# Optimization experiments

Hardware: AMD Instinct MI355X
Metric: run time of the kernel (lower is better)

The kernel has to match this reference:

```python
import jax, jax.numpy as jnp
import numpy as np

EPS = 1e-20


def setup_inputs() -> dict:
    key = jax.random.key(0)
    k_u, k_w = jax.random.split(key)
    B, n_in, d_in, N, D = 128, 1152, 8, 32, 16
    u = jax.random.normal(k_u, (B, n_in, d_in), dtype=jnp.float32)
    # xavier_normal for W: fan_in = d_in, fan_out = D (last two dims)
    std = float(np.sqrt(2.0 / (d_in + D)))
    W = jax.random.normal(k_w, (n_in, N, d_in, D), dtype=jnp.float32) * std
    b = jnp.zeros((n_in, N), dtype=jnp.float32)
    return {"u": u, "W": W, "b": b}


def reference(u, W, b):
    # u: [B, i, n]; W: [i, j, n, m]; u_hat: [B, i, j, m]
    u_hat = jnp.einsum('ijnm,bin->bijm', W, u)
    # agreement score uses detached (stop-gradient) u_hat
    u_hat_d = jax.lax.stop_gradient(u_hat)
    D = W.shape[-1]
    a = jnp.einsum('bijm,bijm->bij', u_hat_d, u_hat_d) / jnp.sqrt(jnp.float32(D))
    # softmax over parent-capsule axis j, plus learned bias b[i, j]
    c = jax.nn.softmax(a, axis=2) + b[None, :, :]
    s = jnp.einsum('bij,bijm->bjm', c, u_hat)
    # squash nonlinearity
    n = jnp.linalg.norm(s, axis=-1, keepdims=True)
    v = (n * n / (1.0 + n * n) / (n + EPS)) * s
    return v
```

## Files before the change

### kernel.cpp

```cpp
#include <hip/hip_runtime.h>
#include <math.h>


#define NB 128
#define NI 1152
#define NJ 32
#define DM 16
#define JMSZ 512
#define BB 4
#define TPB 256
#define BPB ((TPB / 64) * BB)

template <int IC_, bool ATOMIC>
__global__ __launch_bounds__(TPB, 4) void caps_main(
    const float* __restrict__ u, const float* __restrict__ W,
    const float* __restrict__ bias, float* __restrict__ out, int nchunk) {
  const int chunk = blockIdx.x;
  const int bg = blockIdx.y;
  const int tid = threadIdx.x;
  const int wid = __builtin_amdgcn_readfirstlane(tid >> 6);
  const int lane = tid & 63;
  const int j = lane >> 1;
  const int h = lane & 1;
  const int b0 = __builtin_amdgcn_readfirstlane(bg * BPB + wid * BB);
  const int i0 = chunk * IC_;

  float acc[BB][8];
#pragma unroll
  for (int bb = 0; bb < BB; ++bb)
#pragma unroll
    for (int k = 0; k < 8; ++k) acc[bb][k] = 0.f;

  const char* wbase = (const char*)W + (size_t)i0 * 16384 + j * 512 + h * 32;

  for (int t = 0; t < IC_; ++t) {
    const int i = i0 + t;
    const char* wp = wbase + (size_t)t * 16384;

    float un[BB][8];
#pragma unroll
    for (int bb = 0; bb < BB; ++bb) {
      const float* up = u + ((size_t)(b0 + bb) * NI + i) * 8;
      float4 a0 = *(const float4*)up;
      float4 a1 = *(const float4*)(up + 4);
      un[bb][0] = a0.x; un[bb][1] = a0.y; un[bb][2] = a0.z; un[bb][3] = a0.w;
      un[bb][4] = a1.x; un[bb][5] = a1.y; un[bb][6] = a1.z; un[bb][7] = a1.w;
    }
    const float bj = bias[(size_t)i * NJ + j];

    float uh[BB][8];
#pragma unroll
    for (int bb = 0; bb < BB; ++bb)
#pragma unroll
      for (int k = 0; k < 8; ++k) uh[bb][k] = 0.f;

#pragma unroll
    for (int half = 0; half < 2; ++half) {
      float4 w0[4], w1[4];
#pragma unroll
      for (int nn = 0; nn < 4; ++nn) {
        const int n = half * 4 + nn;
        w0[nn] = *(const float4*)(wp + n * 64);
        w1[nn] = *(const float4*)(wp + n * 64 + 16);
      }
#pragma unroll
      for (int nn = 0; nn < 4; ++nn) {
        const int n = half * 4 + nn;
#pragma unroll
        for (int bb = 0; bb < BB; ++bb) {
          const float uv = un[bb][n];
          uh[bb][0] = fmaf(uv, w0[nn].x, uh[bb][0]);
          uh[bb][1] = fmaf(uv, w0[nn].y, uh[bb][1]);
          uh[bb][2] = fmaf(uv, w0[nn].z, uh[bb][2]);
          uh[bb][3] = fmaf(uv, w0[nn].w, uh[bb][3]);
          uh[bb][4] = fmaf(uv, w1[nn].x, uh[bb][4]);
          uh[bb][5] = fmaf(uv, w1[nn].y, uh[bb][5]);
          uh[bb][6] = fmaf(uv, w1[nn].z, uh[bb][6]);
          uh[bb][7] = fmaf(uv, w1[nn].w, uh[bb][7]);
        }
      }
    }

    float s2[BB], e[BB], es[BB];
#pragma unroll
    for (int bb = 0; bb < BB; ++bb) {
      float v = uh[bb][0] * uh[bb][0];
#pragma unroll
      for (int k = 1; k < 8; ++k) v = fmaf(uh[bb][k], uh[bb][k], v);
      s2[bb] = v;
    }
#pragma unroll
    for (int bb = 0; bb < BB; ++bb) s2[bb] += __shfl_xor(s2[bb], 1);
#pragma unroll
    for (int bb = 0; bb < BB; ++bb) e[bb] = __expf(s2[bb] * 0.25f);
#pragma unroll
    for (int bb = 0; bb < BB; ++bb) es[bb] = e[bb];
#pragma unroll
    for (int mask = 2; mask <= 32; mask <<= 1)
#pragma unroll
      for (int bb = 0; bb < BB; ++bb) es[bb] += __shfl_xor(es[bb], mask);
#pragma unroll
    for (int bb = 0; bb < BB; ++bb) {
      const float c = e[bb] * __builtin_amdgcn_rcpf(es[bb]) + bj;
#pragma unroll
      for (int k = 0; k < 8; ++k) acc[bb][k] = fmaf(c, uh[bb][k], acc[bb][k]);
    }
  }

#pragma unroll
  for (int bb = 0; bb < BB; ++bb) {
    if (ATOMIC) {
      float* p = out + (size_t)(b0 + bb) * JMSZ + j * DM + h * 8;
#pragma unroll
      for (int k = 0; k < 8; ++k) atomicAdd(p + k, acc[bb][k]);
    } else {
      float* p = out + ((size_t)(b0 + bb) * nchunk + chunk) * JMSZ + j * DM + h * 8;
      *(float4*)p = make_float4(acc[bb][0], acc[bb][1], acc[bb][2], acc[bb][3]);
      *(float4*)(p + 4) = make_float4(acc[bb][4], acc[bb][5], acc[bb][6], acc[bb][7]);
    }
  }
}

template <int NSUM>
__global__ __launch_bounds__(256) void caps_fin(const float* __restrict__ part,
                                                float* __restrict__ v) {
  if constexpr (NSUM == 1) {
    const int o = blockIdx.x * 256 + threadIdx.x;
    const float s = part[o];
    float sq = s * s;
    sq += __shfl_xor(sq, 1);
    sq += __shfl_xor(sq, 2);
    sq += __shfl_xor(sq, 4);
    sq += __shfl_xor(sq, 8);
    const float nrm = sqrtf(sq);
    v[o] = (sq / (1.0f + sq)) / (nrm + 1e-20f) * s;
  } else {
    constexpr int QC = NSUM / 8;
    const int lane = threadIdx.x & 63;
    const int wv = (blockIdx.x * 256 + threadIdx.x) >> 6;
    const int q = lane >> 3;
    const int r = lane & 7;
    const int F = wv * 8 + r;
    const int b = F >> 7;
    const int jm4 = F & 127;
    const float* p = part + (size_t)b * NSUM * JMSZ + (size_t)q * QC * JMSZ + jm4 * 4;
    float4 s4 = make_float4(0.f, 0.f, 0.f, 0.f);
#pragma unroll 4
    for (int cc = 0; cc < QC; ++cc) {
      float4 x = *(const float4*)(p + (size_t)cc * JMSZ);
      s4.x += x.x; s4.y += x.y; s4.z += x.z; s4.w += x.w;
    }
#pragma unroll
    for (int mask = 8; mask <= 32; mask <<= 1) {
      s4.x += __shfl_xor(s4.x, mask);
      s4.y += __shfl_xor(s4.y, mask);
      s4.z += __shfl_xor(s4.z, mask);
      s4.w += __shfl_xor(s4.w, mask);
    }
    float sq = s4.x * s4.x + s4.y * s4.y + s4.z * s4.z + s4.w * s4.w;
    sq += __shfl_xor(sq, 1);
    sq += __shfl_xor(sq, 2);
    const float nrm = sqrtf(sq);
    const float f = (sq / (1.0f + sq)) / (nrm + 1e-20f);
    if (q == 0)
      *(float4*)(v + (size_t)F * 4) = make_float4(f * s4.x, f * s4.y, f * s4.z, f * s4.w);
  }
}

extern "C" void kernel_launch(void* const* d_in, const int* in_sizes, int n_in,
                              void* d_out, int out_size, void* d_ws, size_t ws_size,
                              hipStream_t stream) {
  const float* u = (const float*)d_in[0];
  const float* W = (const float*)d_in[1];
  const float* bias = (const float*)d_in[2];
  float* out = (float*)d_out;

  const size_t P128 = (size_t)NB * 128 * JMSZ * sizeof(float);
  const size_t P64 = (size_t)NB * 64 * JMSZ * sizeof(float);

  if (ws_size >= P128) {
    float* part = (float*)d_ws;
    caps_main<9, false><<<dim3(128, NB / BPB), TPB, 0, stream>>>(u, W, bias, part, 128);
    caps_fin<128><<<512, 256, 0, stream>>>(part, out);
  } else if (ws_size >= P64) {
    float* part = (float*)d_ws;
    caps_main<18, false><<<dim3(64, NB / BPB), TPB, 0, stream>>>(u, W, bias, part, 64);
    caps_fin<64><<<512, 256, 0, stream>>>(part, out);
  } else {
    float* sbuf = (float*)d_ws;
    hipMemsetAsync(sbuf, 0, (size_t)NB * JMSZ * sizeof(float), stream);
    caps_main<18, true><<<dim3(64, NB / BPB), TPB, 0, stream>>>(u, W, bias, sbuf, 64);
    caps_fin<1><<<(NB * JMSZ) / 256, 256, 0, stream>>>(sbuf, out);
  }
}
```

Before: 111.7 us.

## Store per-chunk partial sums as bf16 and split input axis into more chunks

The main kernel now writes its per-chunk partial capsule sums to the workspace as bf16 instead of fp32, halving partial-buffer traffic. The reduction kernel reads 8 bf16 values per lane and accumulates in fp32. The chunk count rises from 128 to 192 (6 inputs per chunk) and occupancy hint goes from 4 to 6, giving more blocks and shorter per-block loops. The cost is bf16 rounding error in each partial sum, which may matter for tolerance checks.

```diff
diff --git a/kernel.cpp b/kernel.cpp
--- a/kernel.cpp
+++ b/kernel.cpp
@@ -1,4 +1,5 @@
 #include <hip/hip_runtime.h>
+#include <hip/hip_bf16.h>
 #include <math.h>
 
 
@@ -11,10 +12,22 @@
 #define TPB 256
 #define BPB ((TPB / 64) * BB)
 
+typedef unsigned short u16;
+typedef u16 u16x8 __attribute__((ext_vector_type(8)));
+
+__device__ __forceinline__ u16 f2bf(float x) {
+  __hip_bfloat16 h = __float2bfloat16(x);
+  return *reinterpret_cast<u16*>(&h);
+}
+__device__ __forceinline__ float bf2f(u16 u) {
+  unsigned int b = ((unsigned int)u) << 16;
+  return __builtin_bit_cast(float, b);
+}
+
 template <int IC_, bool ATOMIC>
-__global__ __launch_bounds__(TPB, 4) void caps_main(
+__global__ __launch_bounds__(TPB, 6) void caps_main(
     const float* __restrict__ u, const float* __restrict__ W,
-    const float* __restrict__ bias, float* __restrict__ out, int nchunk) {
+    const float* __restrict__ bias, void* __restrict__ outv, int nchunk) {
   const int chunk = blockIdx.x;
   const int bg = blockIdx.y;
   const int tid = threadIdx.x;
@@ -110,21 +123,24 @@
 #pragma unroll
   for (int bb = 0; bb < BB; ++bb) {
     if (ATOMIC) {
-      float* p = out + (size_t)(b0 + bb) * JMSZ + j * DM + h * 8;
+      float* p = (float*)outv + (size_t)(b0 + bb) * JMSZ + j * DM + h * 8;
 #pragma unroll
       for (int k = 0; k < 8; ++k) atomicAdd(p + k, acc[bb][k]);
     } else {
-      float* p = out + ((size_t)(b0 + bb) * nchunk + chunk) * JMSZ + j * DM + h * 8;
-      *(float4*)p = make_float4(acc[bb][0], acc[bb][1], acc[bb][2], acc[bb][3]);
-      *(float4*)(p + 4) = make_float4(acc[bb][4], acc[bb][5], acc[bb][6], acc[bb][7]);
+      u16* p = (u16*)outv + ((size_t)(b0 + bb) * nchunk + chunk) * JMSZ + j * DM + h * 8;
+      u16x8 o8;
+#pragma unroll
+      for (int k = 0; k < 8; ++k) o8[k] = f2bf(acc[bb][k]);
+      *(u16x8*)p = o8;
     }
   }
 }
 
 template <int NSUM>
-__global__ __launch_bounds__(256) void caps_fin(const float* __restrict__ part,
+__global__ __launch_bounds__(256) void caps_fin(const void* __restrict__ partv,
                                                 float* __restrict__ v) {
   if constexpr (NSUM == 1) {
+    const float* part = (const float*)partv;
     const int o = blockIdx.x * 256 + threadIdx.x;
     const float s = part[o];
     float sq = s * s;
@@ -135,35 +151,40 @@
     const float nrm = sqrtf(sq);
     v[o] = (sq / (1.0f + sq)) / (nrm + 1e-20f) * s;
   } else {
+    const u16* part = (const u16*)partv;
     constexpr int QC = NSUM / 8;
     const int lane = threadIdx.x & 63;
     const int wv = (blockIdx.x * 256 + threadIdx.x) >> 6;
     const int q = lane >> 3;
     const int r = lane & 7;
     const int F = wv * 8 + r;
-    const int b = F >> 7;
-    const int jm4 = F & 127;
-    const float* p = part + (size_t)b * NSUM * JMSZ + (size_t)q * QC * JMSZ + jm4 * 4;
-    float4 s4 = make_float4(0.f, 0.f, 0.f, 0.f);
+    const int b = F >> 6;
+    const int jm8 = F & 63;
+    const u16* p = part + (size_t)b * NSUM * JMSZ + (size_t)q * QC * JMSZ + jm8 * 8;
+    float s[8];
+#pragma unroll
+    for (int k = 0; k < 8; ++k) s[k] = 0.f;
 #pragma unroll 4
     for (int cc = 0; cc < QC; ++cc) {
-      float4 x = *(const float4*)(p + (size_t)cc * JMSZ);
-      s4.x += x.x; s4.y += x.y; s4.z += x.z; s4.w += x.w;
-    }
-#pragma unroll
-    for (int mask = 8; mask <= 32; mask <<= 1) {
-      s4.x += __shfl_xor(s4.x, mask);
-      s4.y += __shfl_xor(s4.y, mask);
-      s4.z += __shfl_xor(s4.z, mask);
-      s4.w += __shfl_xor(s4.w, mask);
-    }
-    float sq = s4.x * s4.x + s4.y * s4.y + s4.z * s4.z + s4.w * s4.w;
+      u16x8 x = *(const u16x8*)(p + (size_t)cc * JMSZ);
+#pragma unroll
+      for (int k = 0; k < 8; ++k) s[k] += bf2f(x[k]);
+    }
+#pragma unroll
+    for (int mask = 8; mask <= 32; mask <<= 1)
+#pragma unroll
+      for (int k = 0; k < 8; ++k) s[k] += __shfl_xor(s[k], mask);
+    float sq = s[0] * s[0];
+#pragma unroll
+    for (int k = 1; k < 8; ++k) sq = fmaf(s[k], s[k], sq);
     sq += __shfl_xor(sq, 1);
-    sq += __shfl_xor(sq, 2);
     const float nrm = sqrtf(sq);
     const float f = (sq / (1.0f + sq)) / (nrm + 1e-20f);
-    if (q == 0)
-      *(float4*)(v + (size_t)F * 4) = make_float4(f * s4.x, f * s4.y, f * s4.z, f * s4.w);
+    if (q == 0) {
+      float* vp = v + (size_t)F * 8;
+      *(float4*)vp = make_float4(f * s[0], f * s[1], f * s[2], f * s[3]);
+      *(float4*)(vp + 4) = make_float4(f * s[4], f * s[5], f * s[6], f * s[7]);
+    }
   }
 }
 
@@ -175,17 +196,15 @@
   const float* bias = (const float*)d_in[2];
   float* out = (float*)d_out;
 
-  const size_t P128 = (size_t)NB * 128 * JMSZ * sizeof(float);
-  const size_t P64 = (size_t)NB * 64 * JMSZ * sizeof(float);
-
-  if (ws_size >= P128) {
-    float* part = (float*)d_ws;
-    caps_main<9, false><<<dim3(128, NB / BPB), TPB, 0, stream>>>(u, W, bias, part, 128);
-    caps_fin<128><<<512, 256, 0, stream>>>(part, out);
-  } else if (ws_size >= P64) {
-    float* part = (float*)d_ws;
-    caps_main<18, false><<<dim3(64, NB / BPB), TPB, 0, stream>>>(u, W, bias, part, 64);
-    caps_fin<64><<<512, 256, 0, stream>>>(part, out);
+  const size_t P192 = (size_t)NB * 192 * JMSZ * sizeof(u16);
+  const size_t P96 = (size_t)NB * 96 * JMSZ * sizeof(u16);
+
+  if (ws_size >= P192) {
+    caps_main<6, false><<<dim3(192, NB / BPB), TPB, 0, stream>>>(u, W, bias, d_ws, 192);
+    caps_fin<192><<<256, 256, 0, stream>>>(d_ws, out);
+  } else if (ws_size >= P96) {
+    caps_main<12, false><<<dim3(96, NB / BPB), TPB, 0, stream>>>(u, W, bias, d_ws, 96);
+    caps_fin<96><<<256, 256, 0, stream>>>(d_ws, out);
   } else {
     float* sbuf = (float*)d_ws;
     hipMemsetAsync(sbuf, 0, (size_t)NB * JMSZ * sizeof(float), stream);
```

Result: slower. 132.3 us (+18.5%).
